# Optimization experiments

Hardware: AMD Instinct MI355X
Metric: run time of the kernel (lower is better)

The kernel has to match this reference:

```python
import jax, jax.numpy as jnp
import numpy as np

# Model dims (see ModelArgs: d_model=1024, expand=2, d_state=16, dt_rank=ceil(1024/16), d_conv=4)
D_MODEL = 1024
D_INNER = 2048
D_STATE = 16
DT_RANK = 64
D_CONV = 4
N_LAYER = 2
VOCAB = 50280  # 50277 padded to multiple of 8
B, L = 1, 1024
EPS = 1e-5


def setup_inputs() -> dict:
    key = jax.random.key(0)
    ks = jax.random.split(key, 12)
    nrm = lambda k, shape, s: (jax.random.normal(k, shape) * s).astype(jnp.float32)
    A = jnp.tile(jnp.arange(1, D_STATE + 1, dtype=jnp.float32), (N_LAYER, D_INNER, 1))
    return {
        "input_ids": jax.random.randint(ks[0], (B, L), 0, VOCAB, dtype=jnp.int32),
        "embedding": nrm(ks[1], (VOCAB, D_MODEL), 0.02),
        "norm_scale": jnp.ones((N_LAYER, D_MODEL), jnp.float32) + nrm(ks[2], (N_LAYER, D_MODEL), 0.02),
        "in_proj_w": nrm(ks[3], (N_LAYER, D_MODEL, 2 * D_INNER), D_MODEL ** -0.5),
        "conv_w": nrm(ks[4], (N_LAYER, D_CONV, D_INNER), D_CONV ** -0.5),
        "conv_b": nrm(ks[5], (N_LAYER, D_INNER), 0.02),
        "x_proj_w": nrm(ks[6], (N_LAYER, D_INNER, DT_RANK + 2 * D_STATE), D_INNER ** -0.5),
        "dt_proj_w": nrm(ks[7], (N_LAYER, DT_RANK, D_INNER), DT_RANK ** -0.5),
        "dt_proj_b": nrm(ks[8], (N_LAYER, D_INNER), 0.02),
        "A_log": jnp.log(A),
        "D_skip": jnp.ones((N_LAYER, D_INNER), jnp.float32),
        "out_proj_w": nrm(ks[9], (N_LAYER, D_INNER, D_MODEL), D_INNER ** -0.5),
        "norm_f_scale": jnp.ones((D_MODEL,), jnp.float32),
    }


def _rmsnorm(x, scale):
    return x * jax.lax.rsqrt(jnp.mean(jnp.square(x), axis=-1, keepdims=True) + EPS) * scale


def _selective_scan(u, delta, A, Bm, Cm, Dp):
    # u, delta: [b,l,d]; A: [d,n]; Bm, Cm: [b,l,n]; Dp: [d]
    deltaA = jnp.exp(jnp.einsum('bld,dn->bldn', delta, A))          # [b,l,d,n]
    dBu = jnp.einsum('bld,bln,bld->bldn', delta, Bm, u)             # [b,l,d,n]

    def step(h, xs):
        dA_t, dBu_t, C_t = xs                                       # [b,d,n],[b,d,n],[b,n]
        h = dA_t * h + dBu_t
        return h, jnp.einsum('bdn,bn->bd', h, C_t)

    h0 = jnp.zeros((u.shape[0], u.shape[2], A.shape[1]), u.dtype)
    _, ys = jax.lax.scan(step, h0, (jnp.swapaxes(deltaA, 0, 1),
                                    jnp.swapaxes(dBu, 0, 1),
                                    jnp.swapaxes(Cm, 0, 1)))
    y = jnp.swapaxes(ys, 0, 1)                                      # [b,l,d]
    return y + u * Dp


def _mamba_block(x, in_w, cw, cb, xp_w, dt_w, dt_b, A_log, Dp, out_w):
    xr = x @ in_w                                                   # [b,l,2*d_inner], no bias
    xc, res = xr[..., :D_INNER], xr[..., D_INNER:]
    # depthwise causal conv: flax pads (K-1) both sides then takes [:, :l] == left-pad K-1
    k = cw[:, None, :]                                              # [K, 1, d_inner] (WIO)
    xc = jax.lax.conv_general_dilated(
        xc, k, window_strides=(1,), padding=[(D_CONV - 1, 0)],
        dimension_numbers=('NWC', 'WIO', 'NWC'), feature_group_count=D_INNER) + cb
    xc = jax.nn.silu(xc)
    A = -jnp.exp(A_log)
    x_dbl = xc @ xp_w                                               # [b,l,dt_rank+2n]
    dt = x_dbl[..., :DT_RANK]
    Bm = x_dbl[..., DT_RANK:DT_RANK + D_STATE]
    Cm = x_dbl[..., DT_RANK + D_STATE:]
    delta = jax.nn.softplus(dt @ dt_w + dt_b)                       # [b,l,d_inner]
    y = _selective_scan(xc, delta, A, Bm, Cm, Dp)
    y = y * jax.nn.silu(res)
    return y @ out_w


def reference(input_ids, embedding, norm_scale, in_proj_w, conv_w, conv_b,
              x_proj_w, dt_proj_w, dt_proj_b, A_log, D_skip, out_proj_w, norm_f_scale):
    x = embedding[input_ids]                                        # [b,l,d_model]

    def layer(x, lp):
        ns, in_w, cw, cb, xpw, dtw, dtb, al, dp, ow = lp
        return x + _mamba_block(_rmsnorm(x, ns), in_w, cw, cb, xpw, dtw, dtb, al, dp, ow), None

    x, _ = jax.lax.scan(layer, x, (norm_scale, in_proj_w, conv_w, conv_b, x_proj_w,
                                   dt_proj_w, dt_proj_b, A_log, D_skip, out_proj_w))
    x = _rmsnorm(x, norm_f_scale)
    return x @ embedding.T                                          # tied lm_head (embedding.attend)
```

## Files before the change

### kernel.cpp

```cpp
#include <hip/hip_runtime.h>

#define DM    1024
#define DI    2048
#define DS    16
#define DTR   64
#define DCONV 4
#define NLAY  2
#define NVOCAB 50280
#define SEQ   1024
#define REPS  1e-5f

typedef unsigned short u16;
typedef short bf16x8 __attribute__((ext_vector_type(8)));
typedef float f32x4 __attribute__((ext_vector_type(4)));

__device__ __forceinline__ u16 bf16_rn(float f) {
  unsigned int u = __float_as_uint(f);
  return (u16)((u + 0x7fffu + ((u >> 16) & 1u)) >> 16);
}
__device__ __forceinline__ float bf16_to_f(u16 h) {
  return __uint_as_float((unsigned int)h << 16);
}
__device__ __forceinline__ float silu_f(float x) { return x / (1.f + __expf(-x)); }

__global__ void k_embed(const int* __restrict__ ids, const float* __restrict__ E,
                        float* __restrict__ x) {
  int t = blockIdx.x;
  int c = threadIdx.x * 4;
  float4 v = *(const float4*)&E[(size_t)ids[t] * DM + c];
  *(float4*)&x[(size_t)t * DM + c] = v;
}

__global__ void k_rmsnorm(const float* __restrict__ x, const float* __restrict__ sc,
                          u16* __restrict__ hi, u16* __restrict__ lo) {
  int t = blockIdx.x, tid = threadIdx.x;
  float4 v = *(const float4*)&x[(size_t)t * DM + tid * 4];
  float s = v.x * v.x + v.y * v.y + v.z * v.z + v.w * v.w;
  for (int o = 32; o; o >>= 1) s += __shfl_xor(s, o);
  __shared__ float red[4];
  if ((tid & 63) == 0) red[tid >> 6] = s;
  __syncthreads();
  float tot = red[0] + red[1] + red[2] + red[3];
  float r = rsqrtf(tot / (float)DM + REPS);
  int c = tid * 4;
  float f[4] = {v.x * r * sc[c + 0], v.y * r * sc[c + 1],
                v.z * r * sc[c + 2], v.w * r * sc[c + 3]};
  unsigned long long ph = 0, pl = 0;
#pragma unroll
  for (int i = 0; i < 4; i++) {
    u16 h = bf16_rn(f[i]);
    u16 l = bf16_rn(f[i] - bf16_to_f(h));
    ph |= (unsigned long long)h << (16 * i);
    pl |= (unsigned long long)l << (16 * i);
  }
  *(unsigned long long*)&hi[(size_t)t * DM + c] = ph;
  *(unsigned long long*)&lo[(size_t)t * DM + c] = pl;
}

struct TDesc { const float* src; u16* dhi; u16* dlo; int R, C, tstart; };
struct TPack { TDesc d[4]; };

__global__ void k_transpose(TPack p) {
  __shared__ float tile[32][33];
  int bt = blockIdx.x;
  int di = 0;
#pragma unroll
  for (int i = 1; i < 4; i++) if (bt >= p.d[i].tstart) di = i;
  TDesc d = p.d[di];
  int tloc = bt - d.tstart;
  int tpc = d.C >> 5;
  int r0 = (tloc / tpc) * 32, c0 = (tloc % tpc) * 32;
  int tx = threadIdx.x & 31, ty = threadIdx.x >> 5;
#pragma unroll
  for (int i = 0; i < 4; i++) {
    int r = ty + i * 8;
    tile[r][tx] = d.src[(size_t)(r0 + r) * d.C + c0 + tx];
  }
  __syncthreads();
#pragma unroll
  for (int i = 0; i < 4; i++) {
    int cr = ty + i * 8;
    float v = tile[tx][cr];
    u16 h = bf16_rn(v);
    size_t off = (size_t)(c0 + cr) * d.R + r0 + tx;
    d.dhi[off] = h;
    d.dlo[off] = bf16_rn(v - bf16_to_f(h));
  }
}

__global__ void k_conv(const float* __restrict__ xr, const float* __restrict__ cw,
                       const float* __restrict__ cb, float* __restrict__ xc) {
  int i = blockIdx.x * 256 + threadIdx.x;
  int t = i >> 11, d = i & (DI - 1);
  float acc = cb[d];
#pragma unroll
  for (int k = 0; k < DCONV; k++) {
    int tt = t - (DCONV - 1) + k;
    if (tt >= 0) acc = fmaf(cw[k * DI + d], xr[(size_t)tt * (2 * DI) + d], acc);
  }
  xc[i] = silu_f(acc);
}

__global__ void k_xdbl(const float* __restrict__ xc, const float* __restrict__ W,
                       float* __restrict__ xdbl) {
  __shared__ float rows[4][DI];
  int t0 = blockIdx.x * 4, tid = threadIdx.x;
#pragma unroll
  for (int it = 0; it < 16; it++) {
    int idx = it * 128 + tid;
    int r = idx >> 9, c = (idx & 511) * 4;
    *(float4*)&rows[r][c] = *(const float4*)&xc[(size_t)(t0 + r) * DI + c];
  }
  __syncthreads();
  int j = tid;
  if (j >= 96) return;
  float acc0 = 0.f, acc1 = 0.f, acc2 = 0.f, acc3 = 0.f;
#pragma unroll 4
  for (int k = 0; k < DI; k++) {
    float w = W[(size_t)k * 96 + j];
    acc0 = fmaf(rows[0][k], w, acc0);
    acc1 = fmaf(rows[1][k], w, acc1);
    acc2 = fmaf(rows[2][k], w, acc2);
    acc3 = fmaf(rows[3][k], w, acc3);
  }
  xdbl[(size_t)(t0 + 0) * 128 + j] = acc0;
  xdbl[(size_t)(t0 + 1) * 128 + j] = acc1;
  xdbl[(size_t)(t0 + 2) * 128 + j] = acc2;
  xdbl[(size_t)(t0 + 3) * 128 + j] = acc3;
}

__global__ void k_dtproj(const float* __restrict__ xdbl, const float* __restrict__ W,
                         const float* __restrict__ b, float* __restrict__ delta) {
  __shared__ float dt[4][DTR];
  int t0 = blockIdx.x * 4;
  int d = blockIdx.y * 256 + threadIdx.x;
  int tid = threadIdx.x;
  {
    int r = tid >> 6, k = tid & 63;
    dt[r][k] = xdbl[(size_t)(t0 + r) * 128 + k];
  }
  __syncthreads();
  float bias = b[d];
  float acc0 = bias, acc1 = bias, acc2 = bias, acc3 = bias;
#pragma unroll
  for (int k = 0; k < DTR; k++) {
    float w = W[(size_t)k * DI + d];
    acc0 = fmaf(dt[0][k], w, acc0);
    acc1 = fmaf(dt[1][k], w, acc1);
    acc2 = fmaf(dt[2][k], w, acc2);
    acc3 = fmaf(dt[3][k], w, acc3);
  }
  float a[4] = {acc0, acc1, acc2, acc3};
#pragma unroll
  for (int r = 0; r < 4; r++) {
    float v = a[r];
    delta[(size_t)(t0 + r) * DI + d] = (v > 20.f) ? v : log1pf(__expf(v));
  }
}

__global__ void k_scan(const float* __restrict__ delta, const float* __restrict__ xdbl,
                       const float* __restrict__ u, const float* __restrict__ A_log,
                       const float* __restrict__ Dskip, float* __restrict__ y) {
  int n = threadIdx.x & 15, dl = threadIdx.x >> 4;
  int d = blockIdx.x * 16 + dl;
  float An = -__expf(A_log[d * DS + n]);
  float Dd = Dskip[d];
  float h = 0.f;
  float del = delta[d], uu = u[d];
  float Bn = xdbl[64 + n], Cn = xdbl[80 + n];
  for (int t = 0; t < SEQ; t++) {
    float del2 = 0.f, uu2 = 0.f, Bn2 = 0.f, Cn2 = 0.f;
    if (t + 1 < SEQ) {
      del2 = delta[(size_t)(t + 1) * DI + d];
      uu2 = u[(size_t)(t + 1) * DI + d];
      Bn2 = xdbl[(t + 1) * 128 + 64 + n];
      Cn2 = xdbl[(t + 1) * 128 + 80 + n];
    }
    float dA = __expf(del * An);
    h = fmaf(dA, h, del * Bn * uu);
    float p = h * Cn;
    p += __shfl_xor(p, 8);
    p += __shfl_xor(p, 4);
    p += __shfl_xor(p, 2);
    p += __shfl_xor(p, 1);
    if (n == 0) y[(size_t)t * DI + d] = fmaf(uu, Dd, p);
    del = del2; uu = uu2; Bn = Bn2; Cn = Cn2;
  }
}

__global__ void k_y2(const float* __restrict__ y, const float* __restrict__ xr,
                     u16* __restrict__ hi, u16* __restrict__ lo) {
  int i = blockIdx.x * 256 + threadIdx.x;
  int t = i >> 11, d = i & (DI - 1);
  float r = xr[(size_t)t * (2 * DI) + DI + d];
  float v = y[i] * silu_f(r);
  u16 h = bf16_rn(v);
  hi[i] = h;
  lo[i] = bf16_rn(v - bf16_to_f(h));
}

#define EPI_STORE 0
#define EPI_ADD 1

__device__ __forceinline__ void async16(const u16* g, u16* l) {
  __builtin_amdgcn_global_load_lds(
      (const __attribute__((address_space(1))) unsigned int*)g,
      (__attribute__((address_space(3))) unsigned int*)l, 16, 0, 0);
}

__device__ __forceinline__ int xcd_swz(int bx, int nwg) {
  return (bx & 7) * (nwg >> 3) + (bx >> 3);
}

template <int EPI, bool BF32, bool NGUARD>
__launch_bounds__(256)
__global__ void k_gemm(const u16* __restrict__ A, const void* __restrict__ Bt,
                       float* __restrict__ C, int M, int N, int K,
                       int ldA, int ldB, int ldC, int Mb) {
  __shared__ u16 lds_a[128 * 32];
  __shared__ u16 lds_b[128 * 32];
  int bx = xcd_swz(blockIdx.x, gridDim.x);
  int m0 = (bx % Mb) * 128;
  int n0 = (bx / Mb) * 128;
  int tid = threadIdx.x, ln = tid & 63;
  int wv = tid >> 6, wm = wv >> 1, wn = wv & 1;
  int ml = ln & 15, q = ln >> 4;

  f32x4 zero = {0.f, 0.f, 0.f, 0.f};
  f32x4 acc[4][4];
#pragma unroll
  for (int i = 0; i < 4; i++)
#pragma unroll
    for (int j = 0; j < 4; j++) acc[i][j] = zero;

  for (int k0 = 0; k0 < K; k0 += 32) {
    __syncthreads();
#pragma unroll
    for (int r = 0; r < 2; r++) {
      int idx = r * 256 + tid;
      const u16* g = A + (size_t)(m0 + (idx >> 2)) * ldA + k0 + (idx & 3) * 8;
      u16* l = lds_a + (size_t)(r * 256 + (tid & ~63)) * 8;
      async16(g, l);
    }
    if (!BF32) {
#pragma unroll
      for (int r = 0; r < 2; r++) {
        int idx = r * 256 + tid;
        const u16* g = (const u16*)Bt + (size_t)(n0 + (idx >> 2)) * ldB + k0 + (idx & 3) * 8;
        u16* l = lds_b + (size_t)(r * 256 + (tid & ~63)) * 8;
        async16(g, l);
      }
    } else {
#pragma unroll
      for (int r = 0; r < 4; r++) {
        int idx = r * 256 + tid;
        int row = idx >> 3, cg = idx & 7;
        int nr = n0 + row;
        if (NGUARD) nr = min(nr, N - 1);
        float4 v = *(const float4*)((const float*)Bt + (size_t)nr * ldB + k0 + cg * 4);
        unsigned long long pk =
            (unsigned long long)bf16_rn(v.x) |
            ((unsigned long long)bf16_rn(v.y) << 16) |
            ((unsigned long long)bf16_rn(v.z) << 32) |
            ((unsigned long long)bf16_rn(v.w) << 48);
        *(unsigned long long*)&lds_b[row * 32 + cg * 4] = pk;
      }
    }
    __syncthreads();

    bf16x8 af[4], bfr[4];
#pragma unroll
    for (int i = 0; i < 4; i++)
      af[i] = *(const bf16x8*)&lds_a[(wm * 64 + i * 16 + ml) * 32 + q * 8];
#pragma unroll
    for (int j = 0; j < 4; j++)
      bfr[j] = *(const bf16x8*)&lds_b[(wn * 64 + j * 16 + ml) * 32 + q * 8];
#pragma unroll
    for (int i = 0; i < 4; i++)
#pragma unroll
      for (int j = 0; j < 4; j++)
        acc[i][j] = __builtin_amdgcn_mfma_f32_16x16x32_bf16(af[i], bfr[j], acc[i][j], 0, 0, 0);
  }

#pragma unroll
  for (int i = 0; i < 4; i++)
#pragma unroll
    for (int j = 0; j < 4; j++) {
      int c = n0 + wn * 64 + j * 16 + ml;
      if (NGUARD && c >= N) continue;
      int rbase = m0 + wm * 64 + i * 16 + q * 4;
#pragma unroll
      for (int rg = 0; rg < 4; rg++) {
        int r = rbase + rg;
        float v = acc[i][j][rg];
        size_t off = (size_t)r * ldC + c;
        if (EPI == EPI_STORE) C[off] = v;
        else C[off] += v;
      }
    }
}

template <int EPI>
__launch_bounds__(256)
__global__ void k_gemm3(const u16* __restrict__ Ah, const u16* __restrict__ Al,
                        const u16* __restrict__ Bh, const u16* __restrict__ Bl,
                        float* __restrict__ C, int M, int N, int K,
                        int ldA, int ldB, int ldC, int Mb) {
  __shared__ u16 lds_ah[128 * 32];
  __shared__ u16 lds_al[128 * 32];
  __shared__ u16 lds_bh[128 * 32];
  __shared__ u16 lds_bl[128 * 32];
  int bx = xcd_swz(blockIdx.x, gridDim.x);
  int m0 = (bx % Mb) * 128;
  int n0 = (bx / Mb) * 128;
  int tid = threadIdx.x, ln = tid & 63;
  int wv = tid >> 6, wm = wv >> 1, wn = wv & 1;
  int ml = ln & 15, q = ln >> 4;

  f32x4 zero = {0.f, 0.f, 0.f, 0.f};
  f32x4 acc[4][4];
#pragma unroll
  for (int i = 0; i < 4; i++)
#pragma unroll
    for (int j = 0; j < 4; j++) acc[i][j] = zero;

  for (int k0 = 0; k0 < K; k0 += 32) {
    __syncthreads();
#pragma unroll
    for (int r = 0; r < 2; r++) {
      int idx = r * 256 + tid;
      size_t goffA = (size_t)(m0 + (idx >> 2)) * ldA + k0 + (idx & 3) * 8;
      size_t goffB = (size_t)(n0 + (idx >> 2)) * ldB + k0 + (idx & 3) * 8;
      size_t loff = (size_t)(r * 256 + (tid & ~63)) * 8;
      async16(Ah + goffA, lds_ah + loff);
      async16(Al + goffA, lds_al + loff);
      async16(Bh + goffB, lds_bh + loff);
      async16(Bl + goffB, lds_bl + loff);
    }
    __syncthreads();

    bf16x8 ah[4], al[4], bh[4], bl[4];
#pragma unroll
    for (int i = 0; i < 4; i++) {
      int ro = (wm * 64 + i * 16 + ml) * 32 + q * 8;
      ah[i] = *(const bf16x8*)&lds_ah[ro];
      al[i] = *(const bf16x8*)&lds_al[ro];
    }
#pragma unroll
    for (int j = 0; j < 4; j++) {
      int ro = (wn * 64 + j * 16 + ml) * 32 + q * 8;
      bh[j] = *(const bf16x8*)&lds_bh[ro];
      bl[j] = *(const bf16x8*)&lds_bl[ro];
    }
#pragma unroll
    for (int i = 0; i < 4; i++)
#pragma unroll
      for (int j = 0; j < 4; j++) {
        acc[i][j] = __builtin_amdgcn_mfma_f32_16x16x32_bf16(ah[i], bh[j], acc[i][j], 0, 0, 0);
        acc[i][j] = __builtin_amdgcn_mfma_f32_16x16x32_bf16(al[i], bh[j], acc[i][j], 0, 0, 0);
        acc[i][j] = __builtin_amdgcn_mfma_f32_16x16x32_bf16(ah[i], bl[j], acc[i][j], 0, 0, 0);
      }
  }

#pragma unroll
  for (int i = 0; i < 4; i++)
#pragma unroll
    for (int j = 0; j < 4; j++) {
      int c = n0 + wn * 64 + j * 16 + ml;
      int rbase = m0 + wm * 64 + i * 16 + q * 4;
#pragma unroll
      for (int rg = 0; rg < 4; rg++) {
        int r = rbase + rg;
        float v = acc[i][j][rg];
        size_t off = (size_t)r * ldC + c;
        if (EPI == EPI_STORE) C[off] = v;
        else C[off] += v;
      }
    }
}

extern "C" void kernel_launch(void* const* d_in, const int* in_sizes, int n_in,
                              void* d_out, int out_size, void* d_ws, size_t ws_size,
                              hipStream_t stream) {
  const int* ids = (const int*)d_in[0];
  const float* E = (const float*)d_in[1];
  const float* norm_scale = (const float*)d_in[2];
  const float* in_proj_w = (const float*)d_in[3];
  const float* conv_w = (const float*)d_in[4];
  const float* conv_b = (const float*)d_in[5];
  const float* x_proj_w = (const float*)d_in[6];
  const float* dt_proj_w = (const float*)d_in[7];
  const float* dt_proj_b = (const float*)d_in[8];
  const float* A_log = (const float*)d_in[9];
  const float* D_skip = (const float*)d_in[10];
  const float* out_proj_w = (const float*)d_in[11];
  const float* norm_f_scale = (const float*)d_in[12];
  float* out = (float*)d_out;

  char* p = (char*)d_ws;
  auto alloc = [&](size_t bytes) { char* r = p; p += (bytes + 255) & ~(size_t)255; return r; };
  float* x = (float*)alloc((size_t)SEQ * DM * 4);
  u16* xn_h = (u16*)alloc((size_t)SEQ * DM * 2);
  u16* xn_l = (u16*)alloc((size_t)SEQ * DM * 2);
  float* xr = (float*)alloc((size_t)SEQ * 2 * DI * 4);
  float* xc = (float*)alloc((size_t)SEQ * DI * 4);
  float* xdbl = (float*)alloc((size_t)SEQ * 128 * 4);
  float* delta = (float*)alloc((size_t)SEQ * DI * 4);
  float* ybuf = (float*)alloc((size_t)SEQ * DI * 4);
  u16* y2h = (u16*)alloc((size_t)SEQ * DI * 2);
  u16* y2l = (u16*)alloc((size_t)SEQ * DI * 2);
  u16* xf_h = (u16*)alloc((size_t)SEQ * DM * 2);
  u16* xf_l = (u16*)alloc((size_t)SEQ * DM * 2);
  u16 *inTh[NLAY], *inTl[NLAY], *outTh[NLAY], *outTl[NLAY];
  for (int l = 0; l < NLAY; l++) {
    inTh[l] = (u16*)alloc((size_t)(2 * DI) * DM * 2);
    inTl[l] = (u16*)alloc((size_t)(2 * DI) * DM * 2);
    outTh[l] = (u16*)alloc((size_t)DM * DI * 2);
    outTl[l] = (u16*)alloc((size_t)DM * DI * 2);
  }

  TPack pk;
  int ts = 0;
  for (int l = 0; l < NLAY; l++) {
    pk.d[l * 2 + 0] = {in_proj_w + (size_t)l * DM * 2 * DI, inTh[l], inTl[l], DM, 2 * DI, ts};
    ts += (DM / 32) * (2 * DI / 32);
    pk.d[l * 2 + 1] = {out_proj_w + (size_t)l * DI * DM, outTh[l], outTl[l], DI, DM, ts};
    ts += (DI / 32) * (DM / 32);
  }
  k_transpose<<<ts, 256, 0, stream>>>(pk);

  k_embed<<<SEQ, 256, 0, stream>>>(ids, E, x);

  for (int l = 0; l < NLAY; l++) {
    k_rmsnorm<<<SEQ, 256, 0, stream>>>(x, norm_scale + (size_t)l * DM, xn_h, xn_l);
    k_gemm3<EPI_STORE><<<8 * 32, 256, 0, stream>>>(
        xn_h, xn_l, inTh[l], inTl[l], xr, SEQ, 2 * DI, DM, DM, DM, 2 * DI, 8);
    k_conv<<<(SEQ * DI) / 256, 256, 0, stream>>>(
        xr, conv_w + (size_t)l * DCONV * DI, conv_b + (size_t)l * DI, xc);
    k_xdbl<<<SEQ / 4, 128, 0, stream>>>(xc, x_proj_w + (size_t)l * DI * 96, xdbl);
    {
      dim3 g(SEQ / 4, DI / 256);
      k_dtproj<<<g, 256, 0, stream>>>(xdbl, dt_proj_w + (size_t)l * DTR * DI,
                                      dt_proj_b + (size_t)l * DI, delta);
    }
    k_scan<<<DI / 16, 256, 0, stream>>>(delta, xdbl, xc,
                                        A_log + (size_t)l * DI * DS,
                                        D_skip + (size_t)l * DI, ybuf);
    k_y2<<<(SEQ * DI) / 256, 256, 0, stream>>>(ybuf, xr, y2h, y2l);
    k_gemm3<EPI_ADD><<<8 * 8, 256, 0, stream>>>(
        y2h, y2l, outTh[l], outTl[l], x, SEQ, DM, DI, DI, DI, DM, 8);
  }

  k_rmsnorm<<<SEQ, 256, 0, stream>>>(x, norm_f_scale, xf_h, xf_l);
  int nblk = (NVOCAB + 127) / 128;
  k_gemm<EPI_STORE, true, true><<<8 * nblk, 256, 0, stream>>>(
      xf_h, E, out, SEQ, NVOCAB, DM, DM, DM, NVOCAB, 8);
}
```

Before: 2.066 ms.

## Pre-convert embedding to bf16, split-K out_proj, and deepen scan prefetch

Adds a kernel that converts the fp32 embedding table to bf16 once, so the lm_head GEMM can use async bf16 loads for B instead of converting fp32 to bf16 inside every tile. The out_proj GEMM is split four ways along K into partial buffers that a new add kernel sums into the residual, which gives more workgroups than the original 64. The selective scan now uses 128-thread blocks and an 8-step register prefetch ring to hide load latency. In exchange it needs extra workspace for the bf16 table and the partials, adds a full pass over the embedding, and launches two more kernels.

Result: faster. 1.906 ms (-7.8%).

```diff
diff --git a/kernel.cpp b/kernel.cpp
--- a/kernel.cpp
+++ b/kernel.cpp
@@ -29,6 +29,18 @@
   int c = threadIdx.x * 4;
   float4 v = *(const float4*)&E[(size_t)ids[t] * DM + c];
   *(float4*)&x[(size_t)t * DM + c] = v;
+}
+
+__global__ void k_e2bf(const float* __restrict__ E, u16* __restrict__ Eb) {
+  size_t i = ((size_t)blockIdx.x * 256 + threadIdx.x) * 8;
+  float4 a = *(const float4*)&E[i];
+  float4 b = *(const float4*)&E[i + 4];
+  union { u16 s[8]; float4 v; } o;
+  o.s[0] = bf16_rn(a.x); o.s[1] = bf16_rn(a.y);
+  o.s[2] = bf16_rn(a.z); o.s[3] = bf16_rn(a.w);
+  o.s[4] = bf16_rn(b.x); o.s[5] = bf16_rn(b.y);
+  o.s[6] = bf16_rn(b.z); o.s[7] = bf16_rn(b.w);
+  *(float4*)&Eb[i] = o.v;
 }
 
 __global__ void k_rmsnorm(const float* __restrict__ x, const float* __restrict__ sc,
@@ -158,33 +170,42 @@
   }
 }
 
+#define SPF 8
 __global__ void k_scan(const float* __restrict__ delta, const float* __restrict__ xdbl,
                        const float* __restrict__ u, const float* __restrict__ A_log,
                        const float* __restrict__ Dskip, float* __restrict__ y) {
   int n = threadIdx.x & 15, dl = threadIdx.x >> 4;
-  int d = blockIdx.x * 16 + dl;
+  int d = blockIdx.x * 8 + dl;
   float An = -__expf(A_log[d * DS + n]);
   float Dd = Dskip[d];
   float h = 0.f;
-  float del = delta[d], uu = u[d];
-  float Bn = xdbl[64 + n], Cn = xdbl[80 + n];
-  for (int t = 0; t < SEQ; t++) {
-    float del2 = 0.f, uu2 = 0.f, Bn2 = 0.f, Cn2 = 0.f;
-    if (t + 1 < SEQ) {
-      del2 = delta[(size_t)(t + 1) * DI + d];
-      uu2 = u[(size_t)(t + 1) * DI + d];
-      Bn2 = xdbl[(t + 1) * 128 + 64 + n];
-      Cn2 = xdbl[(t + 1) * 128 + 80 + n];
-    }
-    float dA = __expf(del * An);
-    h = fmaf(dA, h, del * Bn * uu);
-    float p = h * Cn;
-    p += __shfl_xor(p, 8);
-    p += __shfl_xor(p, 4);
-    p += __shfl_xor(p, 2);
-    p += __shfl_xor(p, 1);
-    if (n == 0) y[(size_t)t * DI + d] = fmaf(uu, Dd, p);
-    del = del2; uu = uu2; Bn = Bn2; Cn = Cn2;
+  float del[SPF], uu[SPF], Bn[SPF], Cn[SPF];
+#pragma unroll
+  for (int s = 0; s < SPF; s++) {
+    del[s] = delta[(size_t)s * DI + d];
+    uu[s] = u[(size_t)s * DI + d];
+    Bn[s] = xdbl[s * 128 + 64 + n];
+    Cn[s] = xdbl[s * 128 + 80 + n];
+  }
+  for (int t = 0; t < SEQ; t += SPF) {
+#pragma unroll
+    for (int s = 0; s < SPF; s++) {
+      float dA = __expf(del[s] * An);
+      h = fmaf(dA, h, del[s] * Bn[s] * uu[s]);
+      float p = h * Cn[s];
+      p += __shfl_xor(p, 8);
+      p += __shfl_xor(p, 4);
+      p += __shfl_xor(p, 2);
+      p += __shfl_xor(p, 1);
+      if (n == 0) y[(size_t)(t + s) * DI + d] = fmaf(uu[s], Dd, p);
+      int tn = t + SPF + s;
+      if (tn < SEQ) {
+        del[s] = delta[(size_t)tn * DI + d];
+        uu[s] = u[(size_t)tn * DI + d];
+        Bn[s] = xdbl[tn * 128 + 64 + n];
+        Cn[s] = xdbl[tn * 128 + 80 + n];
+      }
+    }
   }
 }
 
@@ -197,6 +218,21 @@
   u16 h = bf16_rn(v);
   hi[i] = h;
   lo[i] = bf16_rn(v - bf16_to_f(h));
+}
+
+__global__ void k_add4(float* __restrict__ x, const float* __restrict__ parts) {
+  int i = (blockIdx.x * 256 + threadIdx.x) * 4;
+  const size_t S = (size_t)SEQ * DM;
+  float4 v = *(const float4*)&x[i];
+  float4 a = *(const float4*)&parts[i];
+  float4 b = *(const float4*)&parts[S + i];
+  float4 c = *(const float4*)&parts[2 * S + i];
+  float4 d = *(const float4*)&parts[3 * S + i];
+  v.x += a.x + b.x + c.x + d.x;
+  v.y += a.y + b.y + c.y + d.y;
+  v.z += a.z + b.z + c.z + d.z;
+  v.w += a.w + b.w + c.w + d.w;
+  *(float4*)&x[i] = v;
 }
 
 #define EPI_STORE 0
@@ -246,7 +282,9 @@
 #pragma unroll
       for (int r = 0; r < 2; r++) {
         int idx = r * 256 + tid;
-        const u16* g = (const u16*)Bt + (size_t)(n0 + (idx >> 2)) * ldB + k0 + (idx & 3) * 8;
+        int nr = n0 + (idx >> 2);
+        if (NGUARD) nr = min(nr, N - 1);
+        const u16* g = (const u16*)Bt + (size_t)nr * ldB + k0 + (idx & 3) * 8;
         u16* l = lds_b + (size_t)(r * 256 + (tid & ~63)) * 8;
         async16(g, l);
       }
@@ -304,15 +342,18 @@
 __launch_bounds__(256)
 __global__ void k_gemm3(const u16* __restrict__ Ah, const u16* __restrict__ Al,
                         const u16* __restrict__ Bh, const u16* __restrict__ Bl,
-                        float* __restrict__ C, int M, int N, int K,
-                        int ldA, int ldB, int ldC, int Mb) {
+                        float* __restrict__ C, int ldA, int ldB, int ldC,
+                        int Mb, int Nb, int kLen, long long cStride) {
   __shared__ u16 lds_ah[128 * 32];
   __shared__ u16 lds_al[128 * 32];
   __shared__ u16 lds_bh[128 * 32];
   __shared__ u16 lds_bl[128 * 32];
   int bx = xcd_swz(blockIdx.x, gridDim.x);
   int m0 = (bx % Mb) * 128;
-  int n0 = (bx / Mb) * 128;
+  int n0 = ((bx / Mb) % Nb) * 128;
+  int sk = bx / (Mb * Nb);
+  int k0beg = sk * kLen;
+  C += (size_t)sk * cStride;
   int tid = threadIdx.x, ln = tid & 63;
   int wv = tid >> 6, wm = wv >> 1, wn = wv & 1;
   int ml = ln & 15, q = ln >> 4;
@@ -324,7 +365,7 @@
 #pragma unroll
     for (int j = 0; j < 4; j++) acc[i][j] = zero;
 
-  for (int k0 = 0; k0 < K; k0 += 32) {
+  for (int k0 = k0beg; k0 < k0beg + kLen; k0 += 32) {
     __syncthreads();
 #pragma unroll
     for (int r = 0; r < 2; r++) {
@@ -411,6 +452,7 @@
   u16* y2l = (u16*)alloc((size_t)SEQ * DI * 2);
   u16* xf_h = (u16*)alloc((size_t)SEQ * DM * 2);
   u16* xf_l = (u16*)alloc((size_t)SEQ * DM * 2);
+  float* parts = (float*)alloc((size_t)4 * SEQ * DM * 4);
   u16 *inTh[NLAY], *inTl[NLAY], *outTh[NLAY], *outTl[NLAY];
   for (int l = 0; l < NLAY; l++) {
     inTh[l] = (u16*)alloc((size_t)(2 * DI) * DM * 2);
@@ -418,6 +460,9 @@
     outTh[l] = (u16*)alloc((size_t)DM * DI * 2);
     outTl[l] = (u16*)alloc((size_t)DM * DI * 2);
   }
+  size_t ebytes = (size_t)NVOCAB * DM * 2;
+  bool useEbf = ((size_t)(p - (char*)d_ws) + ebytes + 256 <= ws_size);
+  u16* Ebf = useEbf ? (u16*)alloc(ebytes) : nullptr;
 
   TPack pk;
   int ts = 0;
@@ -428,13 +473,15 @@
     ts += (DI / 32) * (DM / 32);
   }
   k_transpose<<<ts, 256, 0, stream>>>(pk);
+  if (useEbf)
+    k_e2bf<<<(NVOCAB * DM) / (256 * 8), 256, 0, stream>>>(E, Ebf);
 
   k_embed<<<SEQ, 256, 0, stream>>>(ids, E, x);
 
   for (int l = 0; l < NLAY; l++) {
     k_rmsnorm<<<SEQ, 256, 0, stream>>>(x, norm_scale + (size_t)l * DM, xn_h, xn_l);
     k_gemm3<EPI_STORE><<<8 * 32, 256, 0, stream>>>(
-        xn_h, xn_l, inTh[l], inTl[l], xr, SEQ, 2 * DI, DM, DM, DM, 2 * DI, 8);
+        xn_h, xn_l, inTh[l], inTl[l], xr, DM, DM, 2 * DI, 8, 32, DM, 0);
     k_conv<<<(SEQ * DI) / 256, 256, 0, stream>>>(
         xr, conv_w + (size_t)l * DCONV * DI, conv_b + (size_t)l * DI, xc);
     k_xdbl<<<SEQ / 4, 128, 0, stream>>>(xc, x_proj_w + (size_t)l * DI * 96, xdbl);
@@ -443,16 +490,23 @@
       k_dtproj<<<g, 256, 0, stream>>>(xdbl, dt_proj_w + (size_t)l * DTR * DI,
                                       dt_proj_b + (size_t)l * DI, delta);
     }
-    k_scan<<<DI / 16, 256, 0, stream>>>(delta, xdbl, xc,
-                                        A_log + (size_t)l * DI * DS,
-                                        D_skip + (size_t)l * DI, ybuf);
+    k_scan<<<DI / 8, 128, 0, stream>>>(delta, xdbl, xc,
+                                       A_log + (size_t)l * DI * DS,
+                                       D_skip + (size_t)l * DI, ybuf);
     k_y2<<<(SEQ * DI) / 256, 256, 0, stream>>>(ybuf, xr, y2h, y2l);
-    k_gemm3<EPI_ADD><<<8 * 8, 256, 0, stream>>>(
-        y2h, y2l, outTh[l], outTl[l], x, SEQ, DM, DI, DI, DI, DM, 8);
+    k_gemm3<EPI_STORE><<<8 * 8 * 4, 256, 0, stream>>>(
+        y2h, y2l, outTh[l], outTl[l], parts, DI, DI, DM, 8, 8, DI / 4,
+        (long long)SEQ * DM);
+    k_add4<<<(SEQ * DM) / (4 * 256), 256, 0, stream>>>(x, parts);
   }
 
   k_rmsnorm<<<SEQ, 256, 0, stream>>>(x, norm_f_scale, xf_h, xf_l);
   int nblk = (NVOCAB + 127) / 128;
-  k_gemm<EPI_STORE, true, true><<<8 * nblk, 256, 0, stream>>>(
-      xf_h, E, out, SEQ, NVOCAB, DM, DM, DM, NVOCAB, 8);
-}
+  if (useEbf) {
+    k_gemm<EPI_STORE, false, true><<<8 * nblk, 256, 0, stream>>>(
+        xf_h, Ebf, out, SEQ, NVOCAB, DM, DM, DM, NVOCAB, 8);
+  } else {
+    k_gemm<EPI_STORE, true, true><<<8 * nblk, 256, 0, stream>>>(
+        xf_h, E, out, SEQ, NVOCAB, DM, DM, DM, NVOCAB, 8);
+  }
+}
```
